# Kernel tuning notes

Hardware: AMD Instinct MI355X
Metric: run time of the kernel (lower is better)

## Reference

```python
import jax, jax.numpy as jnp
import numpy as np

K = 3          # kernel_size
PAD = 1        # padding
HEADS = 4
C = 128
K2 = K * K


def setup_inputs() -> dict:
    key = jax.random.key(0)
    k1, k2, k3, k4 = jax.random.split(key, 4)
    B, H, W = 4, 128, 128
    x = jax.random.normal(k1, (B, H, W, C), jnp.float32)
    w_qkv = jax.random.normal(k2, (K2 * K2 * HEADS, C), jnp.float32) * 0.02
    w_v = jax.random.normal(k3, (K2, C, C), jnp.float32) * np.sqrt(2.0 / (K2 * C))
    w_proj = jax.random.normal(k4, (C, C), jnp.float32) * 0.02
    return {"x": x, "w_qkv": w_qkv, "w_v": w_v, "w_proj": w_proj}


def _csa(x, w_qkv, w_v, w_proj):
    B, H, W, Cc = x.shape
    hd = Cc // HEADS
    scale = hd ** (-0.5)
    N = H * W
    # attention map: Linear(C -> k^4*heads); pool is identity for stride=1
    att = jnp.einsum('bhwc,oc->bhwo', x, w_qkv)                      # [B,H,W,81*heads]
    att = att.reshape(B, N, HEADS, K2, K2).transpose(0, 2, 1, 3, 4)  # [B,heads,N,k2,k2]
    att = jax.nn.softmax(att * scale, axis=-1)
    # unfold x into per-location 3x3 windows (patch index p = di*K + dj)
    xp = jnp.pad(x, ((0, 0), (PAD, PAD), (PAD, PAD), (0, 0)))
    patches = jnp.stack([xp[:, di:di + H, dj:dj + W, :]
                         for di in range(K) for dj in range(K)], axis=3)  # [B,H,W,k2,C]
    v = patches.reshape(B, N, K2, Cc)
    # grouped 1x1 conv == per-window-position CxC matmul
    v = jnp.einsum('pij,bnpj->bnpi', w_v, v)                          # [B,N,k2,C]
    v = v.reshape(B, N, K2, HEADS, hd).transpose(0, 3, 1, 2, 4)       # [B,heads,N,k2,hd]
    out = jnp.einsum('bhnpq,bhnqd->bhnpd', att, v)                    # [B,heads,N,k2,hd]
    # -> [B, C, k2, H, W] with channel index = head*hd + d (matches torch fold layout)
    out = out.transpose(0, 1, 4, 3, 2).reshape(B, Cc, K2, H, W)
    # fold: scatter-add overlapping patches back to (H, W)
    acc = jnp.zeros((B, Cc, H + 2 * PAD, W + 2 * PAD), x.dtype)
    p = 0
    for di in range(K):
        for dj in range(K):
            acc = acc.at[:, :, di:di + H, dj:dj + W].add(out[:, :, p])
            p += 1
    y = acc[:, :, PAD:PAD + H, PAD:PAD + W].transpose(0, 2, 3, 1)     # [B,H,W,C]
    return jnp.einsum('bhwc,oc->bhwo', y, w_proj)


def reference(x, w_qkv, w_v, w_proj):
    return _csa(x, w_qkv, w_v, w_proj)
```

## Files before the change

kernel.cpp:

```cpp
#include <hip/hip_runtime.h>


typedef short bf16x8 __attribute__((ext_vector_type(8)));
typedef float f32x4  __attribute__((ext_vector_type(4)));
typedef float v2f    __attribute__((ext_vector_type(2)));

#define SCALE 0.17677669529663687f

__device__ __forceinline__ unsigned short f2bf(float f) {
  unsigned u = __float_as_uint(f);
  u = (u + 0x7fffu + ((u >> 16) & 1u)) >> 16;
  return (unsigned short)u;
}
__device__ __forceinline__ float bf2f(unsigned short s) {
  return __uint_as_float(((unsigned)s) << 16);
}
__device__ __forceinline__ unsigned pk2bf(float lo, float hi) {
  unsigned a = __float_as_uint(lo) + 0x8000u;
  unsigned b = __float_as_uint(hi) + 0x8000u;
  return __builtin_amdgcn_perm(b, a, 0x07060302u);
}
__device__ __forceinline__ bf16x8 ld16(const unsigned short* p) {
  union { bf16x8 v; uint4 u; } r;
  r.u = *(const uint4*)p;
  return r.v;
}

__global__ __launch_bounds__(256) void cvt_kernel(const float* __restrict__ wq,
                                                  const float* __restrict__ wv,
                                                  const float* __restrict__ wp,
                                                  unsigned short* __restrict__ wqb2,
                                                  unsigned short* __restrict__ wvb2,
                                                  unsigned short* __restrict__ wpb2) {
  int i = blockIdx.x * 256 + threadIdx.x;
  if (i >= 26624) return;
  if (i < 6144) {
    int l = i & 63, rest = i >> 6;
    int kk = rest & 3, r2 = rest >> 2;
    int tile = r2 % 6, h = r2 / 6;
    int col = tile * 16 + (l & 15);
    int k0 = kk * 32 + (l >> 4) * 8;
    unsigned short* d = wqb2 + (long)i * 8;
    ushort4 o0 = make_ushort4(0, 0, 0, 0), o1 = make_ushort4(0, 0, 0, 0);
    if (col < 81) {
      const float* s = wq + (long)(h * 81 + col) * 128 + k0;
      float4 a = *(const float4*)s, b = *(const float4*)(s + 4);
      o0.x = f2bf(a.x); o0.y = f2bf(a.y); o0.z = f2bf(a.z); o0.w = f2bf(a.w);
      o1.x = f2bf(b.x); o1.y = f2bf(b.y); o1.z = f2bf(b.z); o1.w = f2bf(b.w);
    }
    *(ushort4*)d = o0;
    *(ushort4*)(d + 4) = o1;
    return;
  }
  const float* s;
  unsigned short* d;
  if (i < 24576) {
    int it = i - 6144;
    int l = it & 63, mk = it >> 6;
    int kk = mk & 3, m = (mk >> 2) & 1, qcg = mk >> 3;
    int cg = qcg & 3, q = qcg >> 2;
    int chan = cg * 32 + m * 16 + (l & 15);
    int k0 = kk * 32 + (l >> 4) * 8;
    s = wv + (long)q * 16384 + chan * 128 + k0;
    d = wvb2 + (long)it * 8;
  } else {
    int it = i - 24576;
    int l = it & 63, kk = (it >> 6) & 3, tn = it >> 8;
    int col = tn * 16 + (l & 15);
    int k0 = kk * 32 + (l >> 4) * 8;
    s = wp + (long)col * 128 + k0;
    d = wpb2 + (long)it * 8;
  }
  float4 a = *(const float4*)s, b = *(const float4*)(s + 4);
  ushort4 o0, o1;
  o0.x = f2bf(a.x); o0.y = f2bf(a.y); o0.z = f2bf(a.z); o0.w = f2bf(a.w);
  o1.x = f2bf(b.x); o1.y = f2bf(b.y); o1.z = f2bf(b.z); o1.w = f2bf(b.w);
  *(ushort4*)d = o0;
  *(ushort4*)(d + 4) = o1;
}

__device__ __forceinline__ void softmax9(const float* L, unsigned short* attile,
                                         int row, int p) {
  float mx = L[0];
#pragma unroll
  for (int q = 1; q < 9; q++) mx = fmaxf(mx, L[q]);
  float e[9], s = 0.f;
#pragma unroll
  for (int q = 0; q < 9; q++) { e[q] = __expf((L[q] - mx) * SCALE); s += e[q]; }
  float inv = 1.f / s;
#pragma unroll
  for (int q = 0; q < 9; q++) attile[row * 90 + q * 10 + p] = f2bf(e[q] * inv);
}

__global__ __launch_bounds__(512, 6) void att_kernel(const float* __restrict__ x,
                                                     const unsigned short* __restrict__ wqb2,
                                                     unsigned* __restrict__ attb) {
  __shared__ unsigned short AT[11520];
  __shared__ float lg[64][84];
  const int t = threadIdx.x;
  const long m0 = (long)blockIdx.x * 64;
#pragma unroll
  for (int k = 0; k < 4; k++) {
    int i = t + k * 512;
    int row = i >> 5, seg = i & 31;
    float4 v = *(const float4*)(x + (m0 + row) * 128 + seg * 4);
    *(uint2*)((unsigned*)AT + row * 68 + seg * 2) =
        make_uint2(pk2bf(v.x, v.y), pk2bf(v.z, v.w));
  }
  const int w = t >> 6, lane = t & 63, qd = lane >> 4, l15 = lane & 15;
  const int rw = w & 3, th = w >> 2;
  const int sr0 = t / 9, sp0 = t - sr0 * 9;
  const int sr1 = (t + 512) / 9, sp1 = (t + 512) - sr1 * 9;
  __syncthreads();
  bf16x8 af[4];
#pragma unroll
  for (int kk = 0; kk < 4; kk++)
    af[kk] = ld16(AT + (rw * 16 + l15) * 136 + kk * 32 + qd * 8);
  const unsigned short* pwb = wqb2 + lane * 8;
  unsigned* ATdw = (unsigned*)AT;

#define STORE_ATT(hh)                                                           \
  { const unsigned* sb = ATdw + ((hh)&1) * 2880;                                \
    _Pragma("unroll") for (int k = 0; k < 6; k++) {                             \
      int i = t + k * 512;                                                      \
      if (i < 2880) {                                                           \
        int q = i / 320, rem = i - q * 320, n = rem / 5, j = rem - n * 5;       \
        attb[((size_t)(q * 4 + (hh)) * 65536 + m0 + n) * 5 + j] =               \
            sb[n * 45 + q * 5 + j];                                             \
      }                                                                         \
    } }

  for (int h = 0; h < 4; h++) {
    f32x4 acc[3] = {};
#pragma unroll
    for (int kk = 0; kk < 4; kk++)
#pragma unroll
      for (int tn = 0; tn < 3; tn++) {
        bf16x8 bf = *(const bf16x8*)(pwb + ((h * 6 + th * 3 + tn) * 4 + kk) * 512);
        acc[tn] = __builtin_amdgcn_mfma_f32_16x16x32_bf16(af[kk], bf, acc[tn], 0, 0, 0);
      }
    __syncthreads();
#pragma unroll
    for (int tn = 0; tn < 3; tn++)
#pragma unroll
      for (int r = 0; r < 4; r++) {
        int col = (th * 3 + tn) * 16 + l15;
        if (col < 81) lg[rw * 16 + qd * 4 + r][col] = acc[tn][r];
      }
    __syncthreads();
    if (h > 0) STORE_ATT(h - 1)
    unsigned short* attile = AT + (h & 1) * 5760;
    softmax9(&lg[sr0][sp0 * 9], attile, sr0, sp0);
    if (t < 64) softmax9(&lg[sr1][sp1 * 9], attile, sr1, sp1);
  }
  __syncthreads();
  STORE_ATT(3)
}

__global__ __launch_bounds__(512, 4) void av_kernel(const float* __restrict__ x,
                                                    const unsigned short* __restrict__ wvb2,
                                                    const unsigned* __restrict__ attb,
                                                    const unsigned short* __restrict__ wpb2,
                                                    float* __restrict__ out) {
  __shared__ unsigned short A[144 * 136];
  __shared__ unsigned short S[100 * 136];
  __shared__ unsigned aLs[2400];
  const int t = threadIdx.x;
  const int bb = blockIdx.z;
  const int r0 = blockIdx.y * 8, c0 = blockIdx.x * 8;
  const int l15 = t & 15, qd = (t >> 4) & 3, wvi = t >> 6;
  const int lane = t & 63;
  const int cg = wvi & 3, lp = wvi >> 2;
  const int n = (wvi & 3) * 16 + l15, lr = n >> 3, lc = n & 7;
  const int g = (wvi >> 2) * 4 + qd, head = g >> 1;
  const long nb = (long)bb * 16384;
  unsigned* Sdw = (unsigned*)S;
  unsigned* Adw = (unsigned*)A;

  int xbI[4];
#pragma unroll
  for (int i = 0; i < 4; i++) {
    int tile = lp * 4 + i;
    int ml = tile < 7 ? tile * 16 + l15 : 0;
    xbI[i] = (ml / 10) * 12 + (ml % 10) + 13;
  }

#pragma unroll
  for (int k = 0; k < 9; k++) {
    int i = t + k * 512;
    int row = i >> 5, seg = i & 31;
    int gr = r0 - 2 + row / 12, gc = c0 - 2 + row % 12;
    float4 v = make_float4(0.f, 0.f, 0.f, 0.f);
    if (gr >= 0 && gr < 128 && gc >= 0 && gc < 128)
      v = *(const float4*)(x + (nb + gr * 128 + gc) * 128 + seg * 4);
    *(uint2*)(Adw + row * 68 + seg * 2) = make_uint2(pk2bf(v.x, v.y), pk2bf(v.z, v.w));
  }

  int aoff[4], aidx[4];
#pragma unroll
  for (int k = 0; k < 4; k++) {
    int i = t + k * 512;
    if (i < 2000) {
      int hh = i / 500, rem = i - hh * 500, row = rem / 5, j5 = rem - row * 5;
      int gr = r0 - 1 + row / 10, gc = c0 - 1 + row % 10;
      aidx[k] = hh * 600 + row * 6 + j5;
      aoff[k] = (gr >= 0 && gr < 128 && gc >= 0 && gc < 128)
                    ? (int)(((size_t)hh * 65536 + nb + gr * 128 + gc) * 5 + j5)
                    : -1;
    } else { aidx[k] = -1; aoff[k] = -1; }
  }
  const unsigned short* pwv = wvb2 + cg * 4096 + lane * 8;

  v2f y2[8];
#pragma unroll
  for (int i = 0; i < 8; i++) y2[i] = (v2f){0.f, 0.f};

  unsigned avv[4];
  bf16x8 wvf[2][4];

#define LOAD_A(qq)                                                              \
  { _Pragma("unroll") for (int k = 0; k < 4; k++)                               \
      avv[k] = (aoff[k] >= 0) ? attb[aoff[k] + (qq) * 1310720] : 0u; }
#define LOAD_WV(qq)                                                             \
  { _Pragma("unroll") for (int m = 0; m < 2; m++)                               \
    _Pragma("unroll") for (int kk = 0; kk < 4; kk++)                            \
      wvf[m][kk] = *(const bf16x8*)(pwv + (size_t)(qq) * 16384 +                \
                                    (m * 4 + kk) * 512); }

  LOAD_A(0)
  LOAD_WV(0)

  for (int q = 0; q < 9; q++) {
    const int qoff = (q / 3) * 12 + (q % 3) - 13;
    __syncthreads();

#pragma unroll
    for (int k = 0; k < 4; k++)
      if (aidx[k] >= 0) aLs[aidx[k]] = avv[k];

#pragma unroll
    for (int i = 0; i < 4; i++) {
      const int tile = lp * 4 + i;
      if (tile < 7) {
        int xr = xbI[i] + qoff;
        xr = xr > 143 ? 143 : xr;
        bf16x8 bx[4];
#pragma unroll
        for (int kk = 0; kk < 4; kk++)
          bx[kk] = ld16(A + xr * 136 + kk * 32 + qd * 8);
        f32x4 acc[2];
#pragma unroll
        for (int m = 0; m < 2; m++) acc[m] = (f32x4){0.f, 0.f, 0.f, 0.f};
#pragma unroll
        for (int kk = 0; kk < 4; kk++)
#pragma unroll
          for (int m = 0; m < 2; m++)
            acc[m] = __builtin_amdgcn_mfma_f32_16x16x32_bf16(wvf[m][kk], bx[kk],
                                                             acc[m], 0, 0, 0);
        int loc = tile * 16 + l15;
        if (loc < 100) {
#pragma unroll
          for (int m = 0; m < 2; m++)
            *(uint2*)(Sdw + loc * 68 + cg * 16 + m * 8 + qd * 2) =
                make_uint2(pk2bf(acc[m][0], acc[m][1]),
                           pk2bf(acc[m][2], acc[m][3]));
        }
      }
    }
    __syncthreads();
    if (q < 8) { LOAD_A(q + 1) LOAD_WV(q + 1) }

    const unsigned short* aS = (const unsigned short*)aLs;
    const int mlb = lr * 10 + lc + 11;
#pragma unroll
    for (int p = 0; p < 9; p++) {
      const int ml = mlb + (1 - p / 3) * 10 + (1 - p % 3);
      const float a = bf2f(aS[head * 1200 + ml * 12 + p]);
      const v2f a2 = {a, a};
      const uint4* Sr = (const uint4*)(Sdw + ml * 68 + g * 8);
#pragma unroll
      for (int v4 = 0; v4 < 2; v4++) {
        const uint4 u = Sr[v4];
        v2f xv;
        const int yi = v4 * 4;
        xv.x = __uint_as_float(u.x << 16); xv.y = __uint_as_float(u.x & 0xffff0000u);
        y2[yi + 0] += a2 * xv;
        xv.x = __uint_as_float(u.y << 16); xv.y = __uint_as_float(u.y & 0xffff0000u);
        y2[yi + 1] += a2 * xv;
        xv.x = __uint_as_float(u.z << 16); xv.y = __uint_as_float(u.z & 0xffff0000u);
        y2[yi + 2] += a2 * xv;
        xv.x = __uint_as_float(u.w << 16); xv.y = __uint_as_float(u.w & 0xffff0000u);
        y2[yi + 3] += a2 * xv;
      }
    }
  }

  __syncthreads();
  unsigned short* yb = A;
  {
    uint4 pk[2];
#pragma unroll
    for (int v4 = 0; v4 < 2; v4++) {
      pk[v4].x = pk2bf(y2[v4 * 4 + 0].x, y2[v4 * 4 + 0].y);
      pk[v4].y = pk2bf(y2[v4 * 4 + 1].x, y2[v4 * 4 + 1].y);
      pk[v4].z = pk2bf(y2[v4 * 4 + 2].x, y2[v4 * 4 + 2].y);
      pk[v4].w = pk2bf(y2[v4 * 4 + 3].x, y2[v4 * 4 + 3].y);
    }
    uint4* dst = (uint4*)(Adw + n * 68 + g * 8);
    dst[0] = pk[0]; dst[1] = pk[1];
  }
  __syncthreads();
  f32x4 pacc[4] = {};
#pragma unroll
  for (int kk = 0; kk < 4; kk++) {
    bf16x8 afr = ld16(yb + ((wvi & 3) * 16 + l15) * 136 + kk * 32 + qd * 8);
#pragma unroll
    for (int tn = 0; tn < 4; tn++) {
      bf16x8 bfr = *(const bf16x8*)(wpb2 + (((wvi >> 2) * 4 + tn) * 4 + kk) * 512 +
                                    lane * 8);
      pacc[tn] = __builtin_amdgcn_mfma_f32_16x16x32_bf16(afr, bfr, pacc[tn], 0, 0, 0);
    }
  }
#pragma unroll
  for (int tn = 0; tn < 4; tn++)
#pragma unroll
    for (int r = 0; r < 4; r++) {
      int nl = (wvi & 3) * 16 + qd * 4 + r;
      int col = ((wvi >> 2) * 4 + tn) * 16 + l15;
      out[(nb + (r0 + (nl >> 3)) * 128 + (c0 + (nl & 7))) * 128 + col] = pacc[tn][r];
    }
}

extern "C" void kernel_launch(void* const* d_in, const int* in_sizes, int n_in,
                              void* d_out, int out_size, void* d_ws, size_t ws_size,
                              hipStream_t stream) {
  const float* x  = (const float*)d_in[0];
  const float* wq = (const float*)d_in[1];
  const float* wv = (const float*)d_in[2];
  const float* wp = (const float*)d_in[3];
  char* w = (char*)d_ws;
  unsigned*       attb = (unsigned*)w;
  unsigned short* wqb2 = (unsigned short*)(w + 47185920);
  unsigned short* wvb2 = wqb2 + 49152;
  unsigned short* wpb2 = wvb2 + 147456;

  cvt_kernel<<<104, 256, 0, stream>>>(wq, wv, wp, wqb2, wvb2, wpb2);
  att_kernel<<<1024, 512, 0, stream>>>(x, wqb2, attb);
  dim3 g3(16, 16, 4);
  av_kernel<<<g3, 512, 0, stream>>>(x, wvb2, attb, wpb2, (float*)d_out);
}
```

Measured before the change: 208.7 us.

## Fuse attention-logit GEMM and softmax into the AV kernel, dropping the global attention buffer

Removes the separate att_kernel and its large global attention buffer. Each av_kernel block now recomputes the softmax attention weights for its 10x10 halo tile with MFMA, from the bf16 input already staged in LDS, and keeps them in a new shared array P. The weight-conversion kernel reorders w_qkv so each MFMA tile maps to patch groups and query positions. The softmax also drops the max subtraction, and weights at out-of-image positions are zeroed through the inverse sum. This trades a global write and read round trip for halo recomputation, much higher LDS use and lower occupancy (launch bounds 512,2), plus overflow risk if the logits grow large.

```diff
diff --git a/kernel.cpp b/kernel.cpp
--- a/kernel.cpp
+++ b/kernel.cpp
@@ -29,22 +29,24 @@
 __global__ __launch_bounds__(256) void cvt_kernel(const float* __restrict__ wq,
                                                   const float* __restrict__ wv,
                                                   const float* __restrict__ wp,
-                                                  unsigned short* __restrict__ wqb2,
+                                                  unsigned short* __restrict__ wq2,
                                                   unsigned short* __restrict__ wvb2,
                                                   unsigned short* __restrict__ wpb2) {
   int i = blockIdx.x * 256 + threadIdx.x;
-  if (i >= 26624) return;
-  if (i < 6144) {
+  if (i >= 27392) return;
+  if (i < 6912) {
     int l = i & 63, rest = i >> 6;
-    int kk = rest & 3, r2 = rest >> 2;
-    int tile = r2 % 6, h = r2 / 6;
-    int col = tile * 16 + (l & 15);
+    int kk = rest & 3, ct = rest >> 2;
+    int s = ct / 3, tile = ct - s * 3;
+    int row16 = l & 15, qd4 = row16 >> 2, r = row16 & 3;
+    int g = s * 4 + qd4, q = tile * 4 + r;
     int k0 = kk * 32 + (l >> 4) * 8;
-    unsigned short* d = wqb2 + (long)i * 8;
+    unsigned short* d = wq2 + (long)i * 8;
     ushort4 o0 = make_ushort4(0, 0, 0, 0), o1 = make_ushort4(0, 0, 0, 0);
-    if (col < 81) {
-      const float* s = wq + (long)(h * 81 + col) * 128 + k0;
-      float4 a = *(const float4*)s, b = *(const float4*)(s + 4);
+    if (q < 9) {
+      int c = (g / 9) * 81 + (g % 9) * 9 + q;
+      const float* sp = wq + (long)c * 128 + k0;
+      float4 a = *(const float4*)sp, b = *(const float4*)(sp + 4);
       o0.x = f2bf(a.x); o0.y = f2bf(a.y); o0.z = f2bf(a.z); o0.w = f2bf(a.w);
       o1.x = f2bf(b.x); o1.y = f2bf(b.y); o1.z = f2bf(b.z); o1.w = f2bf(b.w);
     }
@@ -54,8 +56,8 @@
   }
   const float* s;
   unsigned short* d;
-  if (i < 24576) {
-    int it = i - 6144;
+  if (i < 25344) {
+    int it = i - 6912;
     int l = it & 63, mk = it >> 6;
     int kk = mk & 3, m = (mk >> 2) & 1, qcg = mk >> 3;
     int cg = qcg & 3, q = qcg >> 2;
@@ -64,7 +66,7 @@
     s = wv + (long)q * 16384 + chan * 128 + k0;
     d = wvb2 + (long)it * 8;
   } else {
-    int it = i - 24576;
+    int it = i - 25344;
     int l = it & 63, kk = (it >> 6) & 3, tn = it >> 8;
     int col = tn * 16 + (l & 15);
     int k0 = kk * 32 + (l >> 4) * 8;
@@ -79,92 +81,14 @@
   *(ushort4*)(d + 4) = o1;
 }
 
-__device__ __forceinline__ void softmax9(const float* L, unsigned short* attile,
-                                         int row, int p) {
-  float mx = L[0];
-#pragma unroll
-  for (int q = 1; q < 9; q++) mx = fmaxf(mx, L[q]);
-  float e[9], s = 0.f;
-#pragma unroll
-  for (int q = 0; q < 9; q++) { e[q] = __expf((L[q] - mx) * SCALE); s += e[q]; }
-  float inv = 1.f / s;
-#pragma unroll
-  for (int q = 0; q < 9; q++) attile[row * 90 + q * 10 + p] = f2bf(e[q] * inv);
-}
-
-__global__ __launch_bounds__(512, 6) void att_kernel(const float* __restrict__ x,
-                                                     const unsigned short* __restrict__ wqb2,
-                                                     unsigned* __restrict__ attb) {
-  __shared__ unsigned short AT[11520];
-  __shared__ float lg[64][84];
-  const int t = threadIdx.x;
-  const long m0 = (long)blockIdx.x * 64;
-#pragma unroll
-  for (int k = 0; k < 4; k++) {
-    int i = t + k * 512;
-    int row = i >> 5, seg = i & 31;
-    float4 v = *(const float4*)(x + (m0 + row) * 128 + seg * 4);
-    *(uint2*)((unsigned*)AT + row * 68 + seg * 2) =
-        make_uint2(pk2bf(v.x, v.y), pk2bf(v.z, v.w));
-  }
-  const int w = t >> 6, lane = t & 63, qd = lane >> 4, l15 = lane & 15;
-  const int rw = w & 3, th = w >> 2;
-  const int sr0 = t / 9, sp0 = t - sr0 * 9;
-  const int sr1 = (t + 512) / 9, sp1 = (t + 512) - sr1 * 9;
-  __syncthreads();
-  bf16x8 af[4];
-#pragma unroll
-  for (int kk = 0; kk < 4; kk++)
-    af[kk] = ld16(AT + (rw * 16 + l15) * 136 + kk * 32 + qd * 8);
-  const unsigned short* pwb = wqb2 + lane * 8;
-  unsigned* ATdw = (unsigned*)AT;
-
-#define STORE_ATT(hh)                                                           \
-  { const unsigned* sb = ATdw + ((hh)&1) * 2880;                                \
-    _Pragma("unroll") for (int k = 0; k < 6; k++) {                             \
-      int i = t + k * 512;                                                      \
-      if (i < 2880) {                                                           \
-        int q = i / 320, rem = i - q * 320, n = rem / 5, j = rem - n * 5;       \
-        attb[((size_t)(q * 4 + (hh)) * 65536 + m0 + n) * 5 + j] =               \
-            sb[n * 45 + q * 5 + j];                                             \
-      }                                                                         \
-    } }
-
-  for (int h = 0; h < 4; h++) {
-    f32x4 acc[3] = {};
-#pragma unroll
-    for (int kk = 0; kk < 4; kk++)
-#pragma unroll
-      for (int tn = 0; tn < 3; tn++) {
-        bf16x8 bf = *(const bf16x8*)(pwb + ((h * 6 + th * 3 + tn) * 4 + kk) * 512);
-        acc[tn] = __builtin_amdgcn_mfma_f32_16x16x32_bf16(af[kk], bf, acc[tn], 0, 0, 0);
-      }
-    __syncthreads();
-#pragma unroll
-    for (int tn = 0; tn < 3; tn++)
-#pragma unroll
-      for (int r = 0; r < 4; r++) {
-        int col = (th * 3 + tn) * 16 + l15;
-        if (col < 81) lg[rw * 16 + qd * 4 + r][col] = acc[tn][r];
-      }
-    __syncthreads();
-    if (h > 0) STORE_ATT(h - 1)
-    unsigned short* attile = AT + (h & 1) * 5760;
-    softmax9(&lg[sr0][sp0 * 9], attile, sr0, sp0);
-    if (t < 64) softmax9(&lg[sr1][sp1 * 9], attile, sr1, sp1);
-  }
-  __syncthreads();
-  STORE_ATT(3)
-}
-
-__global__ __launch_bounds__(512, 4) void av_kernel(const float* __restrict__ x,
+__global__ __launch_bounds__(512, 2) void av_kernel(const float* __restrict__ x,
                                                     const unsigned short* __restrict__ wvb2,
-                                                    const unsigned* __restrict__ attb,
+                                                    const unsigned short* __restrict__ wq2,
                                                     const unsigned short* __restrict__ wpb2,
                                                     float* __restrict__ out) {
   __shared__ unsigned short A[144 * 136];
   __shared__ unsigned short S[100 * 136];
-  __shared__ unsigned aLs[2400];
+  __shared__ unsigned P[18100];
   const int t = threadIdx.x;
   const int bb = blockIdx.z;
   const int r0 = blockIdx.y * 8, c0 = blockIdx.x * 8;
@@ -195,48 +119,70 @@
       v = *(const float4*)(x + (nb + gr * 128 + gc) * 128 + seg * 4);
     *(uint2*)(Adw + row * 68 + seg * 2) = make_uint2(pk2bf(v.x, v.y), pk2bf(v.z, v.w));
   }
-
-  int aoff[4], aidx[4];
-#pragma unroll
-  for (int k = 0; k < 4; k++) {
-    int i = t + k * 512;
-    if (i < 2000) {
-      int hh = i / 500, rem = i - hh * 500, row = rem / 5, j5 = rem - row * 5;
-      int gr = r0 - 1 + row / 10, gc = c0 - 1 + row % 10;
-      aidx[k] = hh * 600 + row * 6 + j5;
-      aoff[k] = (gr >= 0 && gr < 128 && gc >= 0 && gc < 128)
-                    ? (int)(((size_t)hh * 65536 + nb + gr * 128 + gc) * 5 + j5)
-                    : -1;
-    } else { aidx[k] = -1; aoff[k] = -1; }
-  }
+  __syncthreads();
+
+#pragma unroll
+  for (int k8 = 0; k8 < 8; k8++) {
+    const int u = wvi * 8 + k8;
+    if (u < 63) {
+      const int s9 = u / 7, lt = u - s9 * 7;
+      const int loc = lt * 16 + l15;
+      const int l10 = loc / 10, lm = loc - l10 * 10;
+      int xr = (l10 + 1) * 12 + lm + 1;
+      xr = xr > 143 ? 143 : xr;
+      bf16x8 bx[4];
+#pragma unroll
+      for (int kk = 0; kk < 4; kk++)
+        bx[kk] = ld16(A + xr * 136 + kk * 32 + qd * 8);
+      f32x4 ac[3];
+#pragma unroll
+      for (int tl = 0; tl < 3; tl++) ac[tl] = (f32x4){0.f, 0.f, 0.f, 0.f};
+      const unsigned short* pq = wq2 + (size_t)s9 * 6144 + lane * 8;
+#pragma unroll
+      for (int tl = 0; tl < 3; tl++)
+#pragma unroll
+        for (int kk = 0; kk < 4; kk++) {
+          bf16x8 aq = *(const bf16x8*)(pq + (tl * 4 + kk) * 512);
+          ac[tl] = __builtin_amdgcn_mfma_f32_16x16x32_bf16(aq, bx[kk], ac[tl], 0, 0, 0);
+        }
+      const int gr = r0 - 1 + l10, gc = c0 - 1 + lm;
+      float e[9], sm = 0.f;
+#pragma unroll
+      for (int q9 = 0; q9 < 9; q9++) {
+        e[q9] = __expf(ac[q9 >> 2][q9 & 3] * SCALE);
+        sm += e[q9];
+      }
+      float inv = (gr >= 0 && gr < 128 && gc >= 0 && gc < 128) ? 1.f / sm : 0.f;
+      if (loc < 100) {
+        unsigned* Pw = P + loc * 181 + (s9 * 4 + qd) * 5;
+        Pw[0] = pk2bf(e[0] * inv, e[1] * inv);
+        Pw[1] = pk2bf(e[2] * inv, e[3] * inv);
+        Pw[2] = pk2bf(e[4] * inv, e[5] * inv);
+        Pw[3] = pk2bf(e[6] * inv, e[7] * inv);
+        Pw[4] = pk2bf(e[8] * inv, 0.f);
+      }
+    }
+  }
+
   const unsigned short* pwv = wvb2 + cg * 4096 + lane * 8;
 
   v2f y2[8];
 #pragma unroll
   for (int i = 0; i < 8; i++) y2[i] = (v2f){0.f, 0.f};
 
-  unsigned avv[4];
   bf16x8 wvf[2][4];
 
-#define LOAD_A(qq)                                                              \
-  { _Pragma("unroll") for (int k = 0; k < 4; k++)                               \
-      avv[k] = (aoff[k] >= 0) ? attb[aoff[k] + (qq) * 1310720] : 0u; }
 #define LOAD_WV(qq)                                                             \
   { _Pragma("unroll") for (int m = 0; m < 2; m++)                               \
     _Pragma("unroll") for (int kk = 0; kk < 4; kk++)                            \
       wvf[m][kk] = *(const bf16x8*)(pwv + (size_t)(qq) * 16384 +                \
                                     (m * 4 + kk) * 512); }
 
-  LOAD_A(0)
   LOAD_WV(0)
 
   for (int q = 0; q < 9; q++) {
     const int qoff = (q / 3) * 12 + (q % 3) - 13;
     __syncthreads();
-
-#pragma unroll
-    for (int k = 0; k < 4; k++)
-      if (aidx[k] >= 0) aLs[aidx[k]] = avv[k];
 
 #pragma unroll
     for (int i = 0; i < 4; i++) {
@@ -268,14 +214,15 @@
       }
     }
     __syncthreads();
-    if (q < 8) { LOAD_A(q + 1) LOAD_WV(q + 1) }
-
-    const unsigned short* aS = (const unsigned short*)aLs;
+    if (q < 8) { LOAD_WV(q + 1) }
+
+    const unsigned short* Ps = (const unsigned short*)P;
     const int mlb = lr * 10 + lc + 11;
+    const int hq = head * 90 + q;
 #pragma unroll
     for (int p = 0; p < 9; p++) {
       const int ml = mlb + (1 - p / 3) * 10 + (1 - p % 3);
-      const float a = bf2f(aS[head * 1200 + ml * 12 + p]);
+      const float a = bf2f(Ps[ml * 362 + hq + p * 10]);
       const v2f a2 = {a, a};
       const uint4* Sr = (const uint4*)(Sdw + ml * 68 + g * 8);
 #pragma unroll
@@ -339,13 +286,11 @@
   const float* wv = (const float*)d_in[2];
   const float* wp = (const float*)d_in[3];
   char* w = (char*)d_ws;
-  unsigned*       attb = (unsigned*)w;
-  unsigned short* wqb2 = (unsigned short*)(w + 47185920);
-  unsigned short* wvb2 = wqb2 + 49152;
+  unsigned short* wq2  = (unsigned short*)w;
+  unsigned short* wvb2 = wq2 + 55296;
   unsigned short* wpb2 = wvb2 + 147456;
 
-  cvt_kernel<<<104, 256, 0, stream>>>(wq, wv, wp, wqb2, wvb2, wpb2);
-  att_kernel<<<1024, 512, 0, stream>>>(x, wqb2, attb);
+  cvt_kernel<<<107, 256, 0, stream>>>(wq, wv, wp, wq2, wvb2, wpb2);
   dim3 g3(16, 16, 4);
-  av_kernel<<<g3, 512, 0, stream>>>(x, wvb2, attb, wpb2, (float*)d_out);
-}
+  av_kernel<<<g3, 512, 0, stream>>>(x, wvb2, wq2, wpb2, (float*)d_out);
+}
```

After: 204.5 us. 2.0% less time.
